# Performance work log

Measured on AMD Instinct MI355X. Metric: run time of the kernel, lower is better.

Reference implementation:

```python
import jax, jax.numpy as jnp
import numpy as np
import math

IN_CH = 512
OUT_CH = 512
K = 3
STYLE_DIM = 512
B, H, W = 8, 64, 64


def setup_inputs() -> dict:
    key = jax.random.key(0)
    k1, k2, k3, k4 = jax.random.split(key, 4)
    return {
        "input": jax.random.normal(k1, (B, IN_CH, H, W), dtype=jnp.float32),
        "style": jax.random.normal(k2, (B, STYLE_DIM), dtype=jnp.float32),
        "weight": jax.random.normal(k3, (1, OUT_CH, IN_CH, K, K), dtype=jnp.float32),
        "mod_weight": jax.random.normal(k4, (IN_CH, STYLE_DIM), dtype=jnp.float32),
        "mod_bias": jnp.ones((IN_CH,), dtype=jnp.float32),
    }


def reference(input, style, weight, mod_weight, mod_bias):
    batch, in_ch, h, w = input.shape
    out_ch = weight.shape[1]
    k = weight.shape[-1]
    conv_scale = 1.0 / math.sqrt(in_ch * k * k)
    lin_scale = 1.0 / math.sqrt(STYLE_DIM)  # EqualLinear scale, lr_mul=1

    # modulation: EqualLinear(style_dim -> in_channel), bias_init=1, no activation
    s = style @ (mod_weight * lin_scale).T + mod_bias  # [B, Cin]

    # per-sample modulated weight: [B, Cout, Cin, K, K]
    wmod = conv_scale * weight * s[:, None, :, None, None]
    demod = jax.lax.rsqrt(jnp.sum(wmod * wmod, axis=(2, 3, 4)) + 1e-8)  # [B, Cout]
    wmod = wmod * demod[:, :, None, None, None]

    # grouped conv with groups = batch (exactly mirrors the torch path)
    lhs = input.reshape(1, batch * in_ch, h, w)
    rhs = wmod.reshape(batch * out_ch, in_ch, k, k)
    pad = (k - 1) // 2
    out = jax.lax.conv_general_dilated(
        lhs, rhs,
        window_strides=(1, 1),
        padding=[(pad, pad), (pad, pad)],
        dimension_numbers=("NCHW", "OIHW", "NCHW"),
        feature_group_count=batch,
    )
    return out.reshape(batch, out_ch, h, w)
```

## Files before the change

kernel.cpp:

```cpp
#include <hip/hip_runtime.h>
#include <hip/hip_bf16.h>
#include <stdint.h>

typedef __attribute__((ext_vector_type(8))) short bf16x8;
typedef __attribute__((ext_vector_type(4))) float f32x4;
typedef __attribute__((ext_vector_type(8))) unsigned short u16x8;

__device__ __forceinline__ unsigned short f2bf(float f) {
  unsigned int u = __float_as_uint(f);
  u = u + 0x7fffu + ((u >> 16) & 1u);
  return (unsigned short)(u >> 16);
}

__global__ void k_sw(const float* __restrict__ style, const float* __restrict__ mw,
                     const float* __restrict__ mb, const float* __restrict__ w,
                     float* __restrict__ s, float* __restrict__ wsq) {
  if (blockIdx.x < 8) {
    __shared__ float st[512];
    const int b = blockIdx.x, t = threadIdx.x;
    st[t]       = style[b*512 + t];
    st[t + 256] = style[b*512 + t + 256];
    __syncthreads();
    for (int k = 0; k < 2; ++k) {
      int c = t + k*256;
      const float* row = mw + (size_t)c * 512;
      float acc = 0.f;
      for (int j = 0; j < 512; ++j) acc += st[j] * row[j];
      s[b*512 + c] = acc * 0.04419417382415922f + mb[c];
    }
  } else {
    int g = (blockIdx.x - 8) * 256 + threadIdx.x;
    const float* p = w + (size_t)g * 9;
    float acc = 0.f;
    #pragma unroll
    for (int t = 0; t < 9; ++t) { float v = p[t]; acc += v*v; }
    wsq[g] = acc;
  }
}

__global__ void k_demod(const float* __restrict__ s, const float* __restrict__ wsq,
                        float* __restrict__ dm) {
  __shared__ float s2[512];
  const int g = blockIdx.x * 256 + threadIdx.x;
  const int b = g >> 9, o = g & 511, t = threadIdx.x;
  float v0 = s[b*512 + t], v1 = s[b*512 + t + 256];
  s2[t] = v0*v0; s2[t+256] = v1*v1;
  __syncthreads();
  const float* row = wsq + (size_t)o * 512;
  float acc = 0.f;
  for (int j = 0; j < 512; ++j) acc += s2[j] * row[j];
  dm[g] = rsqrtf(acc * (1.0f/4608.0f) + 1e-8f);
}

__global__ void k_wt(const float* __restrict__ w, float* __restrict__ wt) {
  const int id = blockIdx.x * 256 + threadIdx.x;
  const int c8 = id & 7, o = (id >> 3) & 511, cb = (id >> 12) & 7, kk = id >> 15;
  const int ci0 = cb*64 + c8*8;
  float v[8];
  #pragma unroll
  for (int e = 0; e < 8; ++e) v[e] = w[((size_t)(o*512 + ci0 + e))*9 + kk];
  float* dst = wt + (((size_t)(kk*8 + cb)*512 + o)*64 + c8*8);
  *(f32x4*)dst       = (f32x4){v[0],v[1],v[2],v[3]};
  *(f32x4*)(dst + 4) = (f32x4){v[4],v[5],v[6],v[7]};
}

__global__ void k_wprep2(const float* __restrict__ wt, const float* __restrict__ s,
                         const float* __restrict__ dm, unsigned short* __restrict__ wp) {
  const int id = blockIdx.x * 256 + threadIdx.x;
  const int b = blockIdx.y;
  const int c8 = id & 7, o = (id >> 3) & 511, cb = (id >> 12) & 7, kk = id >> 15;
  const int ci0 = cb*64 + c8*8;
  const float dmo = 0.014731391274719739f  * dm[b*512 + o];
  f32x4 s0 = *(const f32x4*)(s + b*512 + ci0);
  f32x4 s1 = *(const f32x4*)(s + b*512 + ci0 + 4);
  const float* src = wt + (((size_t)(kk*8 + cb)*512 + o)*64 + c8*8);
  f32x4 w0 = *(const f32x4*)src, w1 = *(const f32x4*)(src + 4);
  u16x8 h;
  #pragma unroll
  for (int e = 0; e < 4; ++e) h[e]     = f2bf(w0[e] * s0[e] * dmo);
  #pragma unroll
  for (int e = 0; e < 4; ++e) h[e + 4] = f2bf(w1[e] * s1[e] * dmo);
  char* base = (char*)wp + ((((size_t)b*9 + kk)*8 + cb)*512 + o)*128
             + ((unsigned)(c8*16) ^ (unsigned)((o & 7) << 4));
  *(u16x8*)base = h;
}

__global__ __launch_bounds__(512, 2) void k_conv(const float* __restrict__ in,
                                                 const unsigned short* __restrict__ wp,
                                                 float* __restrict__ out) {
  __shared__ __align__(16) unsigned char ldsA[3*32768];
  __shared__ __align__(16) unsigned char ldsB[49152];

  const int tid = threadIdx.x;
  const int lan15 = tid & 15;
  const int lgrp = (tid >> 4) & 3;
  const int wid = tid >> 6;
  const int wm = wid >> 2, wn = wid & 3;
  const unsigned wg = blockIdx.x;
  const int b = wg & 7, pt = (wg >> 3) & 15, ot = (wg >> 7) & 1;
  const int o0 = ot * 256, y0 = pt * 4;

  const float* inb = in + (size_t)b * 512 * 4096;
  const unsigned short* wpb = wp + (size_t)b * 9 * 8 * 512 * 64;

  auto stageA = [&](int tap, int cbb, int buf) {
    const char* src = (const char*)(wpb + (((size_t)tap*8 + cbb)*512 + (size_t)o0) * 64);
    unsigned char* dst = ldsA + buf*32768;
    #pragma unroll
    for (int r = 0; r < 4; ++r) {
      __builtin_amdgcn_global_load_lds(
        (const __attribute__((address_space(1))) unsigned int*)(src + tid*16 + r*8192),
        (__attribute__((address_space(3))) unsigned int*)(dst + tid*16 + r*8192),
        16, 0, 0);
    }
  };

  f32x4 bv0[6], bv1[6];
  unsigned bp[6][4];
  auto loadB = [&](int cbb) {
    const int cp = tid & 31, xq = (tid >> 5) & 15;
    #pragma unroll
    for (int j = 0; j < 6; ++j) {
      const int yi = y0 - 1 + j;
      const int yc = yi < 0 ? 0 : (yi > 63 ? 63 : yi);
      const float* p0 = inb + ((size_t)(cbb*64 + cp*2) * 64 + yc) * 64 + xq*4;
      bv0[j] = *(const f32x4*)p0;
      bv1[j] = *(const f32x4*)(p0 + 4096);
    }
  };
  auto convB = [&]() {
    #pragma unroll
    for (int j = 0; j < 6; ++j)
      #pragma unroll
      for (int e = 0; e < 4; ++e)
        bp[j][e] = (unsigned)f2bf(bv0[j][e]) | ((unsigned)f2bf(bv1[j][e]) << 16);
  };
  auto writeB = [&]() {
    const int cp = tid & 31, xq = (tid >> 5) & 15;
    #pragma unroll
    for (int j = 0; j < 6; ++j) {
      const int yi = y0 - 1 + j;
      const bool valid = (yi >= 0) & (yi < 64);
      #pragma unroll
      for (int e = 0; e < 4; ++e) {
        const int x = xq*4 + e;
        *(unsigned*)(ldsB + j*8192 + x*128 + ((cp*4) ^ ((x & 7) << 4))) = valid ? bp[j][e] : 0u;
      }
    }
  };

  f32x4 acc[8][4];
  #pragma unroll
  for (int mf = 0; mf < 8; ++mf)
    #pragma unroll
    for (int nf = 0; nf < 4; ++nf)
      acc[mf][nf] = (f32x4){0.f, 0.f, 0.f, 0.f};

  const int aB0 = (wm*128 + lan15)*128 + ((lgrp*16) ^ ((lan15 & 7) << 4));
  const int aB1 = aB0 ^ 64;
  int cB0[3], cB1[3];
  #pragma unroll
  for (int kx = 0; kx < 3; ++kx) {
    const int x0 = lan15 + kx - 1;
    cB0[kx] = wn*8192 + x0*128 + ((lgrp*16) ^ ((x0 & 7) << 4));
    cB1[kx] = cB0[kx] ^ 64;
  }
  const bool zL = (lan15 == 0), zR = (lan15 == 15);

#define ENDB(N) asm volatile("s_waitcnt vmcnt(" #N ")\n\ts_barrier" ::: "memory")

#define COMPUTE(KK) { \
    constexpr int ky_ = (KK)/3, kx_ = (KK)%3; \
    const unsigned char* Ab = ldsA + ((KK)%3)*32768; \
    __builtin_amdgcn_s_setprio(1); \
    _Pragma("unroll") \
    for (int ks = 0; ks < 2; ++ks) { \
      const int aB = ks ? aB1 : aB0; \
      const int cBk = ks ? cB1[kx_] : cB0[kx_]; \
      bf16x8 af[8], bfr[4]; \
      _Pragma("unroll") \
      for (int mf = 0; mf < 8; ++mf) \
        af[mf] = *(const bf16x8*)(Ab + aB + mf*2048); \
      _Pragma("unroll") \
      for (int nf = 0; nf < 4; ++nf) { \
        bf16x8 v = *(const bf16x8*)(ldsB + ky_*8192 + cBk + nf*2048); \
        if (kx_ == 0 && nf == 0) { if (zL) v = (bf16x8){0,0,0,0,0,0,0,0}; } \
        if (kx_ == 2 && nf == 3) { if (zR) v = (bf16x8){0,0,0,0,0,0,0,0}; } \
        bfr[nf] = v; \
      } \
      _Pragma("unroll") \
      for (int mf = 0; mf < 8; ++mf) \
        _Pragma("unroll") \
        for (int nf = 0; nf < 4; ++nf) \
          acc[mf][nf] = __builtin_amdgcn_mfma_f32_16x16x32_bf16(af[mf], bfr[nf], acc[mf][nf], 0, 0, 0); \
    } \
    __builtin_amdgcn_s_setprio(0); }

#define IT6(KK) { stageA((KK)+2, cb, ((KK)+2)%3); COMPUTE(KK); ENDB(4); }

  loadB(0);
  asm volatile("" ::: "memory");
  stageA(0, 0, 0);
  stageA(1, 0, 1);
  asm volatile("s_waitcnt vmcnt(8)" ::: "memory");
  convB();
  writeB();
  asm volatile("s_waitcnt vmcnt(4) lgkmcnt(0)\n\ts_barrier" ::: "memory");

  for (int cb = 0; cb < 7; ++cb) {
    IT6(0) IT6(1) IT6(2) IT6(3) IT6(4) IT6(5) IT6(6)
    stageA(0, cb + 1, 0);
    asm volatile("" ::: "memory");
    COMPUTE(7);
    loadB(cb + 1);
    ENDB(16);
    asm volatile("s_waitcnt vmcnt(0)" ::: "memory");
    convB();
    stageA(1, cb + 1, 1);
    COMPUTE(8);
    asm volatile("s_barrier" ::: "memory");
    writeB();
    asm volatile("s_waitcnt lgkmcnt(0)\n\ts_barrier" ::: "memory");
  }
  {
    const int cb = 7;
    IT6(0) IT6(1) IT6(2) IT6(3) IT6(4) IT6(5) IT6(6)
    COMPUTE(7); ENDB(0);
    COMPUTE(8);
  }

  float* outb = out + (size_t)b * 512 * 4096;
  #pragma unroll
  for (int mf = 0; mf < 8; ++mf) {
    const int o = o0 + wm*128 + mf*16 + lgrp*4;
    #pragma unroll
    for (int nf = 0; nf < 4; ++nf) {
      const int p = pt*256 + wn*64 + nf*16 + lan15;
      #pragma unroll
      for (int r = 0; r < 4; ++r)
        outb[(size_t)(o + r) * 4096 + p] = acc[mf][nf][r];
    }
  }
#undef IT6
#undef COMPUTE
#undef ENDB
}

extern "C" void kernel_launch(void* const* d_in, const int* in_sizes, int n_in,
                              void* d_out, int out_size, void* d_ws, size_t ws_size,
                              hipStream_t stream) {
  const float* input  = (const float*)d_in[0];
  const float* style  = (const float*)d_in[1];
  const float* weight = (const float*)d_in[2];
  const float* mw     = (const float*)d_in[3];
  const float* mb     = (const float*)d_in[4];
  float* out = (float*)d_out;
  char* ws = (char*)d_ws;
  float* s     = (float*)ws;
  float* demod = (float*)(ws + 16384);
  float* wsq   = (float*)(ws + 32768);
  float* wt    = (float*)(ws + 1081344);
  unsigned short* wp = (unsigned short*)(ws + 10518528);

  hipLaunchKernelGGL(k_wt,     dim3(1152),     dim3(256), 0, stream, weight, wt);
  hipLaunchKernelGGL(k_sw,     dim3(1032),     dim3(256), 0, stream, style, mw, mb, weight, s, wsq);
  hipLaunchKernelGGL(k_demod,  dim3(16),       dim3(256), 0, stream, s, wsq, demod);
  hipLaunchKernelGGL(k_wprep2, dim3(1152, 8),  dim3(256), 0, stream, wt, s, demod, wp);
  hipLaunchKernelGGL(k_conv,   dim3(256),      dim3(512), 0, stream, input, wp, out);
}
```

Baseline: 214.2 us.

## Split each conv tap into four barrier-separated LDS-read/MFMA phases

Each 3x3 tap's compute is restructured into four phases, each loading half the A fragments (and B when needed) and issuing 16 MFMAs. Extra workgroup barriers are placed between phases to keep waves in lockstep, in a ping-pong style. The global-load wait now comes before the tap's compute rather than after it. This cuts the live fragment registers from 12 to 8 vectors and is meant to interleave LDS reads with MFMA work. The cost is four barriers per tap, which could stall waves, and a leftover dead first TAP definition.

```diff
diff --git a/kernel.cpp b/kernel.cpp
--- a/kernel.cpp
+++ b/kernel.cpp
@@ -167,36 +167,51 @@
   }
   const bool zL = (lan15 == 0), zR = (lan15 == 15);
 
-#define ENDB(N) asm volatile("s_waitcnt vmcnt(" #N ")\n\ts_barrier" ::: "memory")
-
-#define COMPUTE(KK) { \
+#define BARR asm volatile("s_barrier" ::: "memory")
+#define GATE(N) asm volatile("s_waitcnt vmcnt(" #N ")\n\ts_barrier" ::: "memory")
+
+#define RD_A(MH, KS) _Pragma("unroll") \
+    for (int i = 0; i < 4; ++i) \
+      af[i] = *(const bf16x8*)(Ab + ((KS) ? aB1 : aB0) + ((MH)*4 + i)*2048);
+
+#define RD_B(KS) _Pragma("unroll") \
+    for (int nf = 0; nf < 4; ++nf) { \
+      bf16x8 v = *(const bf16x8*)(Bb + ((KS) ? cB1[kx_] : cB0[kx_]) + nf*2048); \
+      if (kx_ == 0 && nf == 0) { if (zL) v = (bf16x8){0,0,0,0,0,0,0,0}; } \
+      if (kx_ == 2 && nf == 3) { if (zR) v = (bf16x8){0,0,0,0,0,0,0,0}; } \
+      bfr[nf] = v; }
+
+#define MF16(MH) { __builtin_amdgcn_s_setprio(1); \
+    _Pragma("unroll") for (int i = 0; i < 4; ++i) \
+      _Pragma("unroll") for (int nf = 0; nf < 4; ++nf) \
+        acc[(MH)*4+i][nf] = __builtin_amdgcn_mfma_f32_16x16x32_bf16(af[i], bfr[nf], acc[(MH)*4+i][nf], 0, 0, 0); \
+    __builtin_amdgcn_s_setprio(0); }
+
+#define PH4 \
+    RD_A(0,0) RD_B(0) MF16(0) \
+    RD_A(1,0) BARR; MF16(1) \
+    RD_A(0,1) RD_B(1) BARR; MF16(0) \
+    RD_A(1,1) BARR; MF16(1)
+
+#define TAP(KK) { \
     constexpr int ky_ = (KK)/3, kx_ = (KK)%3; \
     const unsigned char* Ab = ldsA + ((KK)%3)*32768; \
-    __builtin_amdgcn_s_setprio(1); \
-    _Pragma("unroll") \
-    for (int ks = 0; ks < 2; ++ks) { \
-      const int aB = ks ? aB1 : aB0; \
-      const int cBk = ks ? cB1[kx_] : cB0[kx_]; \
-      bf16x8 af[8], bfr[4]; \
-      _Pragma("unroll") \
-      for (int mf = 0; mf < 8; ++mf) \
-        af[mf] = *(const bf16x8*)(Ab + aB + mf*2048); \
-      _Pragma("unroll") \
-      for (int nf = 0; nf < 4; ++nf) { \
-        bf16x8 v = *(const bf16x8*)(ldsB + ky_*8192 + cBk + nf*2048); \
-        if (kx_ == 0 && nf == 0) { if (zL) v = (bf16x8){0,0,0,0,0,0,0,0}; } \
-        if (kx_ == 2 && nf == 3) { if (zR) v = (bf16x8){0,0,0,0,0,0,0,0}; } \
-        bfr[nf] = v; \
-      } \
-      _Pragma("unroll") \
-      for (int mf = 0; mf < 8; ++mf) \
-        _Pragma("unroll") \
-        for (int nf = 0; nf < 4; ++nf) \
-          acc[mf][nf] = __builtin_amdgcn_mfma_f32_16x16x32_bf16(af[mf], bfr[nf], acc[mf][nf], 0, 0, 0); \
-    } \
-    __builtin_amdgcn_s_setprio(0); }
-
-#define IT6(KK) { stageA((KK)+2, cb, ((KK)+2)%3); COMPUTE(KK); ENDB(4); }
+    const unsigned char* Bb = ldsB + ky_*8192 + wn*8192 - wn*8192 + (wn)*0 + (wn + 0)*0 + (wn)*0 + ky_*0; \
+    (void)ky_; \
+    bf16x8 af[4], bfr[4]; \
+    stageA((KK)+2, cb, ((KK)+2)%3); \
+    GATE(8); \
+    PH4 }
+
+#undef TAP
+#define TAP(KK) { \
+    constexpr int ky_ = (KK)/3, kx_ = (KK)%3; \
+    const unsigned char* Ab = ldsA + ((KK)%3)*32768; \
+    const unsigned char* Bb = ldsB + ky_*8192; \
+    bf16x8 af[4], bfr[4]; \
+    stageA((KK)+2, cb, ((KK)+2)%3); \
+    GATE(8); \
+    PH4 }
 
   loadB(0);
   asm volatile("" ::: "memory");
@@ -208,25 +223,50 @@
   asm volatile("s_waitcnt vmcnt(4) lgkmcnt(0)\n\ts_barrier" ::: "memory");
 
   for (int cb = 0; cb < 7; ++cb) {
-    IT6(0) IT6(1) IT6(2) IT6(3) IT6(4) IT6(5) IT6(6)
-    stageA(0, cb + 1, 0);
-    asm volatile("" ::: "memory");
-    COMPUTE(7);
-    loadB(cb + 1);
-    ENDB(16);
-    asm volatile("s_waitcnt vmcnt(0)" ::: "memory");
-    convB();
-    stageA(1, cb + 1, 1);
-    COMPUTE(8);
-    asm volatile("s_barrier" ::: "memory");
-    writeB();
-    asm volatile("s_waitcnt lgkmcnt(0)\n\ts_barrier" ::: "memory");
+    TAP(0) TAP(1) TAP(2) TAP(3) TAP(4) TAP(5) TAP(6)
+    {
+      constexpr int ky_ = 2, kx_ = 1;
+      const unsigned char* Ab = ldsA + (7%3)*32768;
+      const unsigned char* Bb = ldsB + ky_*8192;
+      bf16x8 af[4], bfr[4];
+      stageA(0, cb + 1, 0);
+      GATE(8);
+      loadB(cb + 1);
+      PH4
+    }
+    {
+      asm volatile("s_waitcnt vmcnt(0)" ::: "memory");
+      convB();
+      stageA(1, cb + 1, 1);
+      constexpr int ky_ = 2, kx_ = 2;
+      const unsigned char* Ab = ldsA + (8%3)*32768;
+      const unsigned char* Bb = ldsB + ky_*8192;
+      bf16x8 af[4], bfr[4];
+      PH4
+      BARR;
+      writeB();
+      asm volatile("s_waitcnt lgkmcnt(0)\n\ts_barrier" ::: "memory");
+    }
   }
   {
     const int cb = 7;
-    IT6(0) IT6(1) IT6(2) IT6(3) IT6(4) IT6(5) IT6(6)
-    COMPUTE(7); ENDB(0);
-    COMPUTE(8);
+    TAP(0) TAP(1) TAP(2) TAP(3) TAP(4) TAP(5) TAP(6)
+    {
+      constexpr int ky_ = 2, kx_ = 1;
+      const unsigned char* Ab = ldsA + (7%3)*32768;
+      const unsigned char* Bb = ldsB + ky_*8192;
+      bf16x8 af[4], bfr[4];
+      GATE(4);
+      PH4
+    }
+    {
+      asm volatile("s_waitcnt vmcnt(0)" ::: "memory");
+      constexpr int ky_ = 2, kx_ = 2;
+      const unsigned char* Ab = ldsA + (8%3)*32768;
+      const unsigned char* Bb = ldsB + ky_*8192;
+      bf16x8 af[4], bfr[4];
+      PH4
+    }
   }
 
   float* outb = out + (size_t)b * 512 * 4096;
@@ -241,9 +281,13 @@
         outb[(size_t)(o + r) * 4096 + p] = acc[mf][nf][r];
     }
   }
-#undef IT6
-#undef COMPUTE
-#undef ENDB
+#undef TAP
+#undef PH4
+#undef MF16
+#undef RD_B
+#undef RD_A
+#undef GATE
+#undef BARR
 }
 
 extern "C" void kernel_launch(void* const* d_in, const int* in_sizes, int n_in,
```

New measurement: 197.5 us. 7.8% less time.
